# Kernel tuning notes

Measured on AMD Instinct MI355X. Metric: run time of the kernel, lower is better.

Reference implementation:

```python
import jax, jax.numpy as jnp
import numpy as np

B, T, H = 8, 512, 1024
DC = 8            # concept_dim_total = 6 + 2
DIN = H + DC      # 1032
V, L = 8, 4       # op_vocab_size, prog_len


def setup_inputs() -> dict:
    key = jax.random.key(0)
    ks = jax.random.split(key, 20)
    s = 0.02
    inp = {
        "x": jax.random.normal(ks[0], (B, T, H), dtype=jnp.float32),
        # concept classifier heads
        "W_tt": jax.random.normal(ks[1], (6, H), dtype=jnp.float32) * s,
        "b_tt": jnp.zeros((6,), jnp.float32),
        "W_pol": jax.random.normal(ks[2], (2, H), dtype=jnp.float32) * s,
        "b_pol": jnp.zeros((2,), jnp.float32),
        # program generator
        "W_c2h": jax.random.normal(ks[3], (H, DIN), dtype=jnp.float32) * s,
        "b_c2h": jnp.zeros((H,), jnp.float32),
        "W_ih": jax.random.normal(ks[4], (3 * H, DIN), dtype=jnp.float32) * s,
        "W_hh": jax.random.normal(ks[5], (3 * H, H), dtype=jnp.float32) * s,
        "b_ih": jnp.zeros((3 * H,), jnp.float32),
        "b_hh": jnp.zeros((3 * H,), jnp.float32),
        "W_proj": jax.random.normal(ks[6], (V, H), dtype=jnp.float32) * s,
        "b_proj": jnp.zeros((V,), jnp.float32),
        # op library: num_ops stacked Linear(DIN->H)-GELU-Linear(H->H)
        "W1": jax.random.normal(ks[7], (V, H, DIN), dtype=jnp.float32) * s,
        "b1": jnp.zeros((V, H), jnp.float32),
        "W2": jax.random.normal(ks[8], (V, H, H), dtype=jnp.float32) * s,
        "b2": jnp.zeros((V, H), jnp.float32),
    }
    return inp


def _forward(x, W_tt, b_tt, W_pol, b_pol, W_c2h, b_c2h, W_ih, W_hh, b_ih, b_hh,
             W_proj, b_proj, W1, b1, W2, b2):
    # concept classifier
    tt = x @ W_tt.T + b_tt              # (B,T,6)
    pol = x @ W_pol.T + b_pol           # (B,T,2)
    concept_feats = jnp.concatenate([tt, pol], axis=-1)  # (B,T,8)
    concept_summary = jnp.concatenate([tt.mean(axis=1), pol.mean(axis=1)], axis=-1)  # (B,8)
    pooled = x.mean(axis=1)             # (B,H)
    context = jnp.concatenate([pooled, concept_summary], axis=-1)  # (B,DIN)

    # program generator: GRU with zero inputs, h0 from context (PyTorch gate eqs)
    h0 = context @ W_c2h.T + b_c2h      # (B,H)
    zero_in = jnp.zeros((context.shape[0], DIN), x.dtype)
    gi = zero_in @ W_ih.T + b_ih        # (B,3H); zero-input contribution = bias
    gi_r, gi_z, gi_n = jnp.split(gi, 3, axis=-1)

    def gru_step(h, _):
        gh = h @ W_hh.T + b_hh
        gh_r, gh_z, gh_n = jnp.split(gh, 3, axis=-1)
        r = jax.nn.sigmoid(gi_r + gh_r)
        z = jax.nn.sigmoid(gi_z + gh_z)
        n = jnp.tanh(gi_n + r * gh_n)
        h_new = (1.0 - z) * n + z * h
        return h_new, h_new

    _, hs = jax.lax.scan(gru_step, h0, None, length=L)   # (L,B,H)
    rnn_out = jnp.transpose(hs, (1, 0, 2))               # (B,L,H)
    program_logits = rnn_out @ W_proj.T + b_proj         # (B,L,V)

    # op library: outputs are identical across L, so compute each op once and
    # average the softmax weights over L (exact same math as expand+mean).
    x_aug = jnp.concatenate([x, concept_feats], axis=-1)           # (B,T,DIN)
    hmid = jax.nn.gelu(jnp.einsum('btd,vhd->btvh', x_aug, W1) + b1, approximate=False)
    op_out = jnp.einsum('btvh,voh->btvo', hmid, W2) + b2           # (B,T,V,H)
    w = jax.nn.softmax(program_logits, axis=-1).mean(axis=1)       # (B,V)
    out = jnp.einsum('btvd,bv->btd', op_out, w)                    # (B,T,H)
    return out, program_logits, tt, pol, pooled


def reference(x, W_tt, b_tt, W_pol, b_pol, W_c2h, b_c2h, W_ih, W_hh, b_ih, b_hh,
              W_proj, b_proj, W1, b1, W2, b2):
    return _forward(x, W_tt, b_tt, W_pol, b_pol, W_c2h, b_c2h, W_ih, W_hh,
                    b_ih, b_hh, W_proj, b_proj, W1, b1, W2, b2)
```

## Files before the change

### kernel.cpp

```cpp
#include <hip/hip_runtime.h>
#include <hip/hip_bf16.h>
#include <math.h>

typedef __bf16 bf16;
typedef __bf16 bf16x8 __attribute__((ext_vector_type(8)));
typedef float f32x4 __attribute__((ext_vector_type(4)));


__device__ __forceinline__ float wsum(float v) {
#pragma unroll
  for (int off = 32; off; off >>= 1) v += __shfl_xor(v, off, 64);
  return v;
}

__device__ __forceinline__ void g2l16(const bf16* g, bf16* l) {
  __builtin_amdgcn_global_load_lds(
      (__attribute__((address_space(1))) void*)g,
      (__attribute__((address_space(3))) void*)l, 16, 0, 0);
}

__device__ __forceinline__ bf16x8 pack8(float4 a, float4 b) {
  bf16x8 r;
  r[0] = (bf16)a.x; r[1] = (bf16)a.y; r[2] = (bf16)a.z; r[3] = (bf16)a.w;
  r[4] = (bf16)b.x; r[5] = (bf16)b.y; r[6] = (bf16)b.z; r[7] = (bf16)b.w;
  return r;
}

__global__ void k_cvt(const float* __restrict__ s, bf16* __restrict__ d, long n) {
  long stride = (long)gridDim.x * blockDim.x;
  for (long i = (long)blockIdx.x * blockDim.x + threadIdx.x; i * 8 < n; i += stride) {
    long e = i * 8;
    if (e + 8 <= n) {
      float4 a = *(const float4*)(s + e);
      float4 b = *(const float4*)(s + e + 4);
      *(bf16x8*)(d + e) = pack8(a, b);
    } else {
      for (long j = e; j < n; j++) d[j] = (bf16)s[j];
    }
  }
}

__global__ void k_xext(const float* __restrict__ x, const float* __restrict__ feats,
                       bf16* __restrict__ xbE, int H, int KE, int DC, long BT) {
  int wave = threadIdx.x >> 6, lane = threadIdx.x & 63;
  long m = (long)blockIdx.x * 4 + wave;
  if (m >= BT) return;
  const float* xp = x + m * H;
  bf16* dp = xbE + m * KE;
  for (int e = lane * 8; e + 8 <= H; e += 512) {
    float4 a = *(const float4*)(xp + e);
    float4 b = *(const float4*)(xp + e + 4);
    *(bf16x8*)(dp + e) = pack8(a, b);
  }
  int pad = KE - H;
  if (lane < pad)
    dp[H + lane] = (lane < DC) ? (bf16)feats[m * DC + lane] : (bf16)0.f;
}

__global__ void k_w1ext(const float* __restrict__ W1, bf16* __restrict__ W1bE,
                        int H, int DIN, int KE, int DC, long N2) {
  int wave = threadIdx.x >> 6, lane = threadIdx.x & 63;
  long n = (long)blockIdx.x * 4 + wave;
  if (n >= N2) return;
  const float* sp = W1 + n * DIN;
  bf16* dp = W1bE + n * KE;
  for (int e = lane * 8; e + 8 <= H; e += 512) {
    float4 a = *(const float4*)(sp + e);
    float4 b = *(const float4*)(sp + e + 4);
    *(bf16x8*)(dp + e) = pack8(a, b);
  }
  int pad = KE - H;
  if (lane < pad)
    dp[H + lane] = (lane < DC) ? (bf16)sp[H + lane] : (bf16)0.f;
}

__global__ void k_init(float* __restrict__ outY, const float* __restrict__ wb2,
                       int H, int T, long BT) {
  int wave = threadIdx.x >> 6, lane = threadIdx.x & 63;
  long gm = (long)blockIdx.x * 4 + wave;
  if (gm >= BT) return;
  int b = (int)(gm / T);
  const float* s = wb2 + (size_t)b * H;
  float* d = outY + gm * H;
  for (int e = lane * 4; e + 4 <= H; e += 256)
    *(float4*)(d + e) = *(const float4*)(s + e);
}

template <int DCT>
__global__ void k_feats_t(const float* __restrict__ x,
                          const float* __restrict__ Wtt, const float* __restrict__ btt,
                          const float* __restrict__ Wpol, const float* __restrict__ bpol,
                          float* __restrict__ out_tt, float* __restrict__ out_pol,
                          float* __restrict__ feats,
                          int H, int T, int BT, int C1, int C2) {
  int wave = threadIdx.x >> 6, lane = threadIdx.x & 63;
  int site = blockIdx.x * 4 + wave;
  if (site >= BT) return;
  const float* xp = x + (size_t)site * H;
  const float* wp[DCT];
#pragma unroll
  for (int c = 0; c < DCT; c++)
    wp[c] = (c < C1) ? (Wtt + (size_t)c * H) : (Wpol + (size_t)(c - C1) * H);
  float acc[DCT];
#pragma unroll
  for (int c = 0; c < DCT; c++) acc[c] = 0.f;
  for (int k = lane * 4; k < H; k += 256) {
    float4 xv = *(const float4*)(xp + k);
#pragma unroll
    for (int c = 0; c < DCT; c++) {
      float4 wv4 = *(const float4*)(wp[c] + k);
      acc[c] += xv.x * wv4.x + xv.y * wv4.y + xv.z * wv4.z + xv.w * wv4.w;
    }
  }
#pragma unroll
  for (int c = 0; c < DCT; c++) acc[c] = wsum(acc[c]);
  if (lane == 0) {
#pragma unroll
    for (int c = 0; c < DCT; c++) {
      float val = acc[c] + (c < C1 ? btt[c] : bpol[c - C1]);
      if (c < C1) out_tt[(size_t)site * C1 + c] = val;
      else        out_pol[(size_t)site * C2 + (c - C1)] = val;
      feats[(size_t)site * DCT + c] = val;
    }
  }
}

__global__ void k_feats_g(const float* __restrict__ x,
                          const float* __restrict__ Wtt, const float* __restrict__ btt,
                          const float* __restrict__ Wpol, const float* __restrict__ bpol,
                          float* __restrict__ out_tt, float* __restrict__ out_pol,
                          float* __restrict__ feats,
                          int H, int T, int BT, int C1, int C2) {
  int wave = threadIdx.x >> 6, lane = threadIdx.x & 63;
  int site = blockIdx.x * 4 + wave;
  if (site >= BT) return;
  int DC = C1 + C2;
  const float* xp = x + (size_t)site * H;
  for (int c = 0; c < DC; c++) {
    const float* wr = (c < C1) ? (Wtt + (size_t)c * H) : (Wpol + (size_t)(c - C1) * H);
    float a = 0.f;
    for (int k = lane; k < H; k += 64) a += xp[k] * wr[k];
    a = wsum(a);
    if (lane == 0) {
      float val = a + (c < C1 ? btt[c] : bpol[c - C1]);
      if (c < C1) out_tt[(size_t)site * C1 + c] = val;
      else        out_pol[(size_t)site * C2 + (c - C1)] = val;
      feats[(size_t)site * DC + c] = val;
    }
  }
}

__global__ void k_fsum(const float* __restrict__ feats, float* __restrict__ fsum,
                       int T, int DC, int BDC) {
  int wave = threadIdx.x >> 6, lane = threadIdx.x & 63;
  int r = blockIdx.x * 4 + wave;
  if (r >= BDC) return;
  int b = r / DC, c = r % DC;
  const float* p = feats + ((size_t)b * T) * DC + c;
  float a = 0.f;
  for (int t = lane; t < T; t += 64) a += p[(size_t)t * DC];
  a = wsum(a);
  if (lane == 0) fsum[r] = a / (float)T;
}

__global__ void k_pool(const float* __restrict__ x, float* __restrict__ pooled,
                       int H, int T, int tsplit) {
  int hBlocks = (H + 255) / 256;
  int bs = blockIdx.x / tsplit, ts = blockIdx.x % tsplit;
  int b = bs / hBlocks;
  int h = (bs % hBlocks) * 256 + threadIdx.x;
  if (h >= H) return;
  int tlo = (int)(((long)T * ts) / tsplit), thi = (int)(((long)T * (ts + 1)) / tsplit);
  const float* p = x + (size_t)b * T * H + h;
  float s = 0.f;
  for (int t = tlo; t < thi; t++) s += p[(size_t)t * H];
  atomicAdd(&pooled[(size_t)b * H + h], s / (float)T);
}

__global__ void k_ctx_h0(const float* __restrict__ Wc2h, const float* __restrict__ bc2h,
                         const float* __restrict__ pooled, const float* __restrict__ fmean,
                         float* __restrict__ h0, float* __restrict__ out_pool,
                         int H, int DIN, int B, int DC) {
  int wave = threadIdx.x >> 6, lane = threadIdx.x & 63;
  int r = blockIdx.x * 4 + wave;
  if (r >= B * H) return;
  int b = r / H, j = r % H;
  const float* wrow = Wc2h + (size_t)j * DIN;
  float a = 0.f;
  for (int k = lane; k < DIN; k += 64) {
    float cv = (k < H) ? pooled[(size_t)b * H + k] : fmean[b * DC + (k - H)];
    a += cv * wrow[k];
  }
  a = wsum(a);
  if (lane == 0) {
    h0[r] = a + bc2h[j];
    out_pool[r] = pooled[r];
  }
}

__global__ void k_gru(const float* __restrict__ hin, const float* __restrict__ Whh,
                      const float* __restrict__ bih, const float* __restrict__ bhh,
                      float* __restrict__ hout, float* __restrict__ hsl,
                      int H, int B) {
  int wave = threadIdx.x >> 6, lane = threadIdx.x & 63;
  int r = blockIdx.x * 4 + wave;
  if (r >= B * H) return;
  int b = r / H, j = r % H;
  const float* h = hin + (size_t)b * H;
  const float* w0 = Whh + (size_t)j * H;
  const float* w1 = Whh + (size_t)(H + j) * H;
  const float* w2 = Whh + (size_t)(2 * H + j) * H;
  float ar = 0, az = 0, an = 0;
  for (int k = lane; k < H; k += 64) {
    float hv = h[k];
    ar += hv * w0[k];
    az += hv * w1[k];
    an += hv * w2[k];
  }
  ar = wsum(ar); az = wsum(az); an = wsum(an);
  if (lane == 0) {
    float ghr = ar + bhh[j];
    float ghz = az + bhh[H + j];
    float ghn = an + bhh[2 * H + j];
    float rg = 1.f / (1.f + expf(-(bih[j] + ghr)));
    float zg = 1.f / (1.f + expf(-(bih[H + j] + ghz)));
    float ng = tanhf(bih[2 * H + j] + rg * ghn);
    float hn = (1.f - zg) * ng + zg * h[j];
    hout[r] = hn;
    hsl[r] = hn;
  }
}

__global__ void k_logits(const float* __restrict__ hs, const float* __restrict__ Wproj,
                         const float* __restrict__ bproj, float* __restrict__ logits,
                         float* __restrict__ out_log, int H, int B, int L, int V) {
  int wave = threadIdx.x >> 6, lane = threadIdx.x & 63;
  int r = blockIdx.x * 4 + wave;
  if (r >= B * L * V) return;
  int b = r / (L * V), rem = r % (L * V), l = rem / V, u = rem % V;
  const float* h = hs + ((size_t)l * B + b) * H;
  const float* w = Wproj + (size_t)u * H;
  float a = 0.f;
  for (int k = lane; k < H; k += 64) a += h[k] * w[k];
  a = wsum(a);
  if (lane == 0) {
    a += bproj[u];
    int idx = (b * L + l) * V + u;
    logits[idx] = a;
    out_log[idx] = a;
  }
}

__global__ void k_wmix(const float* __restrict__ logits, const float* __restrict__ b2,
                       float* __restrict__ wv, float* __restrict__ wb2,
                       int B, int L, int V, int H) {
  __shared__ float sm[2048];
  __shared__ float wsh[512];
  int t = threadIdx.x;
  if (t < B * L) {
    const float* lg = logits + t * V;
    float mx = lg[0];
    for (int u = 1; u < V; u++) mx = fmaxf(mx, lg[u]);
    float s = 0.f;
    for (int u = 0; u < V; u++) s += expf(lg[u] - mx);
    for (int u = 0; u < V; u++) sm[t * V + u] = expf(lg[u] - mx) / s;
  }
  __syncthreads();
  if (t < B * V) {
    int b = t / V, u = t % V;
    float a = 0.f;
    for (int l = 0; l < L; l++) a += sm[(b * L + l) * V + u];
    a /= (float)L;
    wsh[t] = a;
    wv[t] = a;
  }
  __syncthreads();
  for (int idx = t; idx < B * H; idx += 256) {
    int b = idx / H, o = idx % H;
    float a = 0.f;
    for (int u = 0; u < V; u++) a += wsh[b * V + u] * b2[(size_t)u * H + o];
    wb2[idx] = a;
  }
}

__global__ __launch_bounds__(256, 2) void gemm1_mfma(
    const bf16* __restrict__ A, const bf16* __restrict__ Bb, bf16* __restrict__ hmid,
    const float* __restrict__ b1, const float* __restrict__ wv,
    int rows, long moff, int KE, int H, int N, int T, int V) {
  __shared__ __align__(16) bf16 As[128 * 32];
  __shared__ __align__(16) bf16 Bs[128 * 32];
  const int wave = threadIdx.x >> 6, lane = threadIdx.x & 63;
  const int m0 = blockIdx.y * 128, n0 = blockIdx.x * 128;
  const int mw = (wave >> 1) * 64, nw = (wave & 1) * 64;
  const int sRow = lane >> 2, sK = (lane & 3) * 8;
  const int rA = lane & 15, q8 = (lane >> 4) * 8;
  f32x4 acc[4][4];
#pragma unroll
  for (int i = 0; i < 4; i++)
#pragma unroll
    for (int j = 0; j < 4; j++) acc[i][j] = (f32x4){0.f, 0.f, 0.f, 0.f};

  int arow[2], brow[2];
#pragma unroll
  for (int t = 0; t < 2; ++t) {
    int s = wave * 2 + t;
    int r = s * 16 + sRow;
    arow[t] = (m0 + r < rows) ? (m0 + r) : (rows - 1);
    brow[t] = (n0 + r < N) ? (n0 + r) : (N - 1);
  }

  for (int k0 = 0; k0 < KE; k0 += 32) {
    __syncthreads();
#pragma unroll
    for (int t = 0; t < 2; ++t) {
      int s = wave * 2 + t;
      g2l16(A + (size_t)arow[t] * KE + k0 + sK, &As[s * 512]);
      g2l16(Bb + (size_t)brow[t] * KE + k0 + sK, &Bs[s * 512]);
    }
    __syncthreads();
    bf16x8 af[4], bf_[4];
#pragma unroll
    for (int i = 0; i < 4; i++) af[i] = *(const bf16x8*)&As[(mw + i * 16 + rA) * 32 + q8];
#pragma unroll
    for (int j = 0; j < 4; j++) bf_[j] = *(const bf16x8*)&Bs[(nw + j * 16 + rA) * 32 + q8];
#pragma unroll
    for (int i = 0; i < 4; i++)
#pragma unroll
      for (int j = 0; j < 4; j++)
        acc[i][j] = __builtin_amdgcn_mfma_f32_16x16x32_bf16(af[i], bf_[j], acc[i][j], 0, 0, 0);
  }

  int vj[4];
  float b1j[4];
#pragma unroll
  for (int j = 0; j < 4; j++) {
    int n = n0 + nw + j * 16 + rA;
    if (n >= N) n = N - 1;
    vj[j] = n / H;
    b1j[j] = b1[n];
  }
#pragma unroll
  for (int i = 0; i < 4; i++) {
#pragma unroll
    for (int r = 0; r < 4; r++) {
      int m = m0 + mw + i * 16 + (lane >> 4) * 4 + r;
      if (m >= rows) continue;
      long gm = moff + m;
      int b = (int)(gm / T);
#pragma unroll
      for (int j = 0; j < 4; j++) {
        int n = n0 + nw + j * 16 + rA;
        if (n >= N) continue;
        float val = acc[i][j][r] + b1j[j];
        val = 0.5f * val * (1.0f + erff(val * 0.70710678118654752f));
        val *= wv[b * V + vj[j]];
        hmid[(size_t)m * N + n] = (bf16)val;
      }
    }
  }
}

__global__ __launch_bounds__(256, 2) void gemm2_mfma(
    const bf16* __restrict__ A, const bf16* __restrict__ W2b, float* __restrict__ outY,
    int rows, long moff, int H, int K, int T, int kchunk) {
  __shared__ __align__(16) bf16 As[128 * 32];
  __shared__ __align__(16) bf16 Bs[128 * 32];
  const int wave = threadIdx.x >> 6, lane = threadIdx.x & 63;
  const int m0 = blockIdx.y * 128, n0 = blockIdx.x * 128;
  const int mw = (wave >> 1) * 64, nw = (wave & 1) * 64;
  const int sRow = lane >> 2, sK = (lane & 3) * 8;
  const int rA = lane & 15, q8 = (lane >> 4) * 8;
  int kz0 = blockIdx.z * kchunk;
  int kz1 = kz0 + kchunk; if (kz1 > K) kz1 = K;
  if (kz0 >= K) return;
  f32x4 acc[4][4];
#pragma unroll
  for (int i = 0; i < 4; i++)
#pragma unroll
    for (int j = 0; j < 4; j++) acc[i][j] = (f32x4){0.f, 0.f, 0.f, 0.f};

  int arow[2], brow[2];
#pragma unroll
  for (int t = 0; t < 2; ++t) {
    int s = wave * 2 + t;
    int r = s * 16 + sRow;
    arow[t] = (m0 + r < rows) ? (m0 + r) : (rows - 1);
    brow[t] = (n0 + r < H) ? (n0 + r) : (H - 1);
  }

  int kv = kz0 / H, kh = kz0 % H;
  for (int k0 = kz0; k0 < kz1; k0 += 32) {
    const bf16* Bk = W2b + (size_t)kv * H * H + kh;
    __syncthreads();
#pragma unroll
    for (int t = 0; t < 2; ++t) {
      int s = wave * 2 + t;
      g2l16(A + (size_t)arow[t] * K + k0 + sK, &As[s * 512]);
      g2l16(Bk + (size_t)brow[t] * H + sK, &Bs[s * 512]);
    }
    __syncthreads();
    bf16x8 af[4], bf_[4];
#pragma unroll
    for (int i = 0; i < 4; i++) af[i] = *(const bf16x8*)&As[(mw + i * 16 + rA) * 32 + q8];
#pragma unroll
    for (int j = 0; j < 4; j++) bf_[j] = *(const bf16x8*)&Bs[(nw + j * 16 + rA) * 32 + q8];
#pragma unroll
    for (int i = 0; i < 4; i++)
#pragma unroll
      for (int j = 0; j < 4; j++)
        acc[i][j] = __builtin_amdgcn_mfma_f32_16x16x32_bf16(af[i], bf_[j], acc[i][j], 0, 0, 0);
    kh += 32;
    if (kh >= H) { kh = 0; kv++; }
  }

#pragma unroll
  for (int i = 0; i < 4; i++) {
#pragma unroll
    for (int r = 0; r < 4; r++) {
      int m = m0 + mw + i * 16 + (lane >> 4) * 4 + r;
      if (m >= rows) continue;
      long gm = moff + m;
#pragma unroll
      for (int j = 0; j < 4; j++) {
        int n = n0 + nw + j * 16 + rA;
        if (n >= H) continue;
        atomicAdd(&outY[(size_t)gm * H + n], acc[i][j][r]);
      }
    }
  }
}

extern "C" void kernel_launch(void* const* d_in, const int* in_sizes, int n_in,
                              void* d_out, int out_size, void* d_ws, size_t ws_size,
                              hipStream_t stream) {
  const float* x      = (const float*)d_in[0];
  const float* W_tt   = (const float*)d_in[1];
  const float* b_tt   = (const float*)d_in[2];
  const float* W_pol  = (const float*)d_in[3];
  const float* b_pol  = (const float*)d_in[4];
  const float* W_c2h  = (const float*)d_in[5];
  const float* b_c2h  = (const float*)d_in[6];
  const float* W_hh   = (const float*)d_in[8];
  const float* b_ih   = (const float*)d_in[9];
  const float* b_hh   = (const float*)d_in[10];
  const float* W_proj = (const float*)d_in[11];
  const float* b_proj = (const float*)d_in[12];
  const float* W1     = (const float*)d_in[13];
  const float* b1     = (const float*)d_in[14];
  const float* W2     = (const float*)d_in[15];
  const float* b2     = (const float*)d_in[16];
  float* out = (float*)d_out;
  char* ws = (char*)d_ws;

  const int C1 = in_sizes[2];
  const int C2 = in_sizes[4];
  const int H  = in_sizes[1] / C1;
  const int DC = C1 + C2;
  const int DIN = H + DC;
  const int V  = in_sizes[12];
  const long BT = (long)in_sizes[0] / H;
  long R = (long)out_size - BT * (long)(H + DC);
  int B = 0, L = 0;
  for (int Lc = 1; Lc <= 32; ++Lc) {
    long den = (long)Lc * V + H;
    if (R % den == 0) {
      long Bc = R / den;
      if (Bc >= 1 && BT % Bc == 0) {
        if (B == 0 || Lc == 4) { B = (int)Bc; L = Lc; }
        if (Lc == 4) break;
      }
    }
  }
  if (B == 0) { B = 8; L = 4; }
  const int T = (int)(BT / B);
  const long N2 = (long)V * H;
  const int KE = H + 32;

  size_t o = 0;
  auto alloc = [&](size_t bytes) { size_t r = o; o = (o + bytes + 255) & ~(size_t)255; return r; };
  float* feats  = (float*)(ws + alloc((size_t)BT * DC * 4));
  size_t off_pooled = alloc((size_t)B * H * 4);
  float* pooled = (float*)(ws + off_pooled);
  size_t off_fsum = alloc((size_t)B * DC * 4);
  float* fsum   = (float*)(ws + off_fsum);
  float* hbuf   = (float*)(ws + alloc((size_t)2 * B * H * 4));
  float* hs     = (float*)(ws + alloc((size_t)L * B * H * 4));
  float* logits = (float*)(ws + alloc((size_t)B * L * V * 4));
  float* wv     = (float*)(ws + alloc((size_t)B * V * 4));
  float* wb2    = (float*)(ws + alloc((size_t)B * H * 4));
  bf16* xbE  = (bf16*)(ws + alloc((size_t)BT * KE * 2));
  bf16* W1bE = (bf16*)(ws + alloc((size_t)N2 * KE * 2));
  bf16* W2b  = (bf16*)(ws + alloc((size_t)N2 * H * 2));
  size_t off_hmid = alloc(0);
  long avail = (long)ws_size - (long)off_hmid;
  long mcMax = avail / (N2 * 2);
  long Mc = (mcMax / 128) * 128;
  long bt128 = ((BT + 127) / 128) * 128;
  if (Mc > bt128) Mc = bt128;
  if (Mc < 128) Mc = 128;
  bf16* hmid = (bf16*)(ws + off_hmid);

  float* out_y    = out;
  float* out_log  = out_y + (size_t)BT * H;
  float* out_tt   = out_log + (size_t)B * L * V;
  float* out_pol  = out_tt + (size_t)BT * C1;
  float* out_pool = out_pol + (size_t)BT * C2;

  hipMemsetAsync(ws + off_pooled, 0, (size_t)B * H * 4, stream);

  k_cvt<<<4096, 256, 0, stream>>>(W2, W2b, N2 * (long)H);
  if (DC == 8 && (H & 1023) == 0)
    k_feats_t<8><<<(int)((BT + 3) / 4), 256, 0, stream>>>(x, W_tt, b_tt, W_pol, b_pol,
                                                          out_tt, out_pol, feats,
                                                          H, T, (int)BT, C1, C2);
  else
    k_feats_g<<<(int)((BT + 3) / 4), 256, 0, stream>>>(x, W_tt, b_tt, W_pol, b_pol,
                                                       out_tt, out_pol, feats,
                                                       H, T, (int)BT, C1, C2);
  k_fsum<<<(B * DC + 3) / 4, 256, 0, stream>>>(feats, fsum, T, DC, B * DC);
  k_xext<<<(int)((BT + 3) / 4), 256, 0, stream>>>(x, feats, xbE, H, KE, DC, BT);
  k_w1ext<<<(int)((N2 + 3) / 4), 256, 0, stream>>>(W1, W1bE, H, DIN, KE, DC, N2);
  int hBlocks = (H + 255) / 256;
  k_pool<<<B * hBlocks * 8, 256, 0, stream>>>(x, pooled, H, T, 8);
  k_ctx_h0<<<(B * H + 3) / 4, 256, 0, stream>>>(W_c2h, b_c2h, pooled, fsum,
                                                hbuf, out_pool, H, DIN, B, DC);
  float* hA = hbuf;
  float* hB = hbuf + (size_t)B * H;
  for (int l = 0; l < L; ++l) {
    k_gru<<<(B * H + 3) / 4, 256, 0, stream>>>((l & 1) ? hB : hA, W_hh, b_ih, b_hh,
                                               (l & 1) ? hA : hB, hs + (size_t)l * B * H,
                                               H, B);
  }
  k_logits<<<(B * L * V + 3) / 4, 256, 0, stream>>>(hs, W_proj, b_proj, logits,
                                                    out_log, H, B, L, V);
  k_wmix<<<1, 256, 0, stream>>>(logits, b2, wv, wb2, B, L, V, H);
  k_init<<<(int)((BT + 3) / 4), 256, 0, stream>>>(out_y, wb2, H, T, BT);

  const int ZS = 4;
  int kchunk = (int)((((N2 / ZS) + 31) / 32) * 32);
  for (long moff = 0; moff < BT; moff += Mc) {
    int rows = (int)(((BT - moff) < Mc) ? (BT - moff) : Mc);
    dim3 g1((unsigned)((N2 + 127) / 128), (unsigned)((rows + 127) / 128));
    dim3 g2((unsigned)((H + 127) / 128), (unsigned)((rows + 127) / 128), ZS);
    gemm1_mfma<<<g1, 256, 0, stream>>>(xbE + (size_t)moff * KE, W1bE, hmid, b1, wv,
                                       rows, moff, KE, H, (int)N2, T, V);
    gemm2_mfma<<<g2, 256, 0, stream>>>(hmid, W2b, out_y,
                                       rows, moff, H, (int)N2, T, kchunk);
  }
}
```

Before: 535.0 us.

## Double GEMM K-tile to 64 with XOR-swizzled LDS, XCD remap, split-K partial buffers

Both MFMA GEMMs now stage 64-wide K tiles into LDS with an XOR swizzle, which halves the number of barrier pairs per K and aims to cut LDS bank conflicts. Block indices are remapped so that tiles sharing operands land on the same XCD, for better L2 reuse. The split-K GEMM2 no longer uses fp32 atomicAdd into the output. It writes per-split partials that a new reduction kernel sums together with the bias term, which replaces the old init kernel. In exchange there is extra workspace and memory traffic for the partials, plus one more launch per chunk. KE padding grows to H+64.

Measured after the change: 459.0 us. -14.2%, faster.

```diff
diff --git a/kernel.cpp b/kernel.cpp
--- a/kernel.cpp
+++ b/kernel.cpp
@@ -72,18 +72,6 @@
   int pad = KE - H;
   if (lane < pad)
     dp[H + lane] = (lane < DC) ? (bf16)sp[H + lane] : (bf16)0.f;
-}
-
-__global__ void k_init(float* __restrict__ outY, const float* __restrict__ wb2,
-                       int H, int T, long BT) {
-  int wave = threadIdx.x >> 6, lane = threadIdx.x & 63;
-  long gm = (long)blockIdx.x * 4 + wave;
-  if (gm >= BT) return;
-  int b = (int)(gm / T);
-  const float* s = wb2 + (size_t)b * H;
-  float* d = outY + gm * H;
-  for (int e = lane * 4; e + 4 <= H; e += 256)
-    *(float4*)(d + e) = *(const float4*)(s + e);
 }
 
 template <int DCT>
@@ -287,47 +275,64 @@
     const bf16* __restrict__ A, const bf16* __restrict__ Bb, bf16* __restrict__ hmid,
     const float* __restrict__ b1, const float* __restrict__ wv,
     int rows, long moff, int KE, int H, int N, int T, int V) {
-  __shared__ __align__(16) bf16 As[128 * 32];
-  __shared__ __align__(16) bf16 Bs[128 * 32];
+  __shared__ __align__(16) bf16 As[128 * 64];
+  __shared__ __align__(16) bf16 Bs[128 * 64];
   const int wave = threadIdx.x >> 6, lane = threadIdx.x & 63;
-  const int m0 = blockIdx.y * 128, n0 = blockIdx.x * 128;
+  int bx = blockIdx.x, by = blockIdx.y;
+  if (gridDim.x == 64 && (gridDim.y & 3) == 0) {
+    int f = by * 64 + bx;
+    int xcd = f & 7, q = f >> 3;
+    int cs = q >> 5, t = q & 31;
+    bx = xcd * 8 + (t & 7);
+    by = cs * 4 + (t >> 3);
+  }
+  const int m0 = by * 128, n0 = bx * 128;
   const int mw = (wave >> 1) * 64, nw = (wave & 1) * 64;
-  const int sRow = lane >> 2, sK = (lane & 3) * 8;
-  const int rA = lane & 15, q8 = (lane >> 4) * 8;
+  const int rr = lane >> 3;
+  const int srcOff = ((lane & 7) ^ rr) << 3;
+  const int rA = lane & 15, q4 = lane >> 4;
   f32x4 acc[4][4];
 #pragma unroll
   for (int i = 0; i < 4; i++)
 #pragma unroll
     for (int j = 0; j < 4; j++) acc[i][j] = (f32x4){0.f, 0.f, 0.f, 0.f};
 
-  int arow[2], brow[2];
-#pragma unroll
-  for (int t = 0; t < 2; ++t) {
-    int s = wave * 2 + t;
-    int r = s * 16 + sRow;
+  int arow[4], brow[4];
+#pragma unroll
+  for (int t = 0; t < 4; ++t) {
+    int r = wave * 32 + t * 8 + rr;
     arow[t] = (m0 + r < rows) ? (m0 + r) : (rows - 1);
     brow[t] = (n0 + r < N) ? (n0 + r) : (N - 1);
   }
 
-  for (int k0 = 0; k0 < KE; k0 += 32) {
+  for (int k0 = 0; k0 < KE; k0 += 64) {
     __syncthreads();
 #pragma unroll
-    for (int t = 0; t < 2; ++t) {
-      int s = wave * 2 + t;
-      g2l16(A + (size_t)arow[t] * KE + k0 + sK, &As[s * 512]);
-      g2l16(Bb + (size_t)brow[t] * KE + k0 + sK, &Bs[s * 512]);
+    for (int t = 0; t < 4; ++t) {
+      int c = wave * 4 + t;
+      g2l16(A + (size_t)arow[t] * KE + k0 + srcOff, &As[c * 512]);
+      g2l16(Bb + (size_t)brow[t] * KE + k0 + srcOff, &Bs[c * 512]);
     }
     __syncthreads();
-    bf16x8 af[4], bf_[4];
-#pragma unroll
-    for (int i = 0; i < 4; i++) af[i] = *(const bf16x8*)&As[(mw + i * 16 + rA) * 32 + q8];
-#pragma unroll
-    for (int j = 0; j < 4; j++) bf_[j] = *(const bf16x8*)&Bs[(nw + j * 16 + rA) * 32 + q8];
-#pragma unroll
-    for (int i = 0; i < 4; i++)
-#pragma unroll
-      for (int j = 0; j < 4; j++)
-        acc[i][j] = __builtin_amdgcn_mfma_f32_16x16x32_bf16(af[i], bf_[j], acc[i][j], 0, 0, 0);
+#pragma unroll
+    for (int kk = 0; kk < 2; ++kk) {
+      bf16x8 af[4], bfr[4];
+#pragma unroll
+      for (int i = 0; i < 4; i++) {
+        int row = mw + i * 16 + rA;
+        af[i] = *(const bf16x8*)&As[row * 64 + ((((kk << 2) + q4) ^ (row & 7)) << 3)];
+      }
+#pragma unroll
+      for (int j = 0; j < 4; j++) {
+        int row = nw + j * 16 + rA;
+        bfr[j] = *(const bf16x8*)&Bs[row * 64 + ((((kk << 2) + q4) ^ (row & 7)) << 3)];
+      }
+#pragma unroll
+      for (int i = 0; i < 4; i++)
+#pragma unroll
+        for (int j = 0; j < 4; j++)
+          acc[i][j] = __builtin_amdgcn_mfma_f32_16x16x32_bf16(af[i], bfr[j], acc[i][j], 0, 0, 0);
+    }
   }
 
   int vj[4];
@@ -343,7 +348,7 @@
   for (int i = 0; i < 4; i++) {
 #pragma unroll
     for (int r = 0; r < 4; r++) {
-      int m = m0 + mw + i * 16 + (lane >> 4) * 4 + r;
+      int m = m0 + mw + i * 16 + q4 * 4 + r;
       if (m >= rows) continue;
       long gm = moff + m;
       int b = (int)(gm / T);
@@ -361,15 +366,24 @@
 }
 
 __global__ __launch_bounds__(256, 2) void gemm2_mfma(
-    const bf16* __restrict__ A, const bf16* __restrict__ W2b, float* __restrict__ outY,
-    int rows, long moff, int H, int K, int T, int kchunk) {
-  __shared__ __align__(16) bf16 As[128 * 32];
-  __shared__ __align__(16) bf16 Bs[128 * 32];
+    const bf16* __restrict__ A, const bf16* __restrict__ W2b, float* __restrict__ part,
+    long partStride, int rows, int H, int K, int kchunk) {
+  __shared__ __align__(16) bf16 As[128 * 64];
+  __shared__ __align__(16) bf16 Bs[128 * 64];
   const int wave = threadIdx.x >> 6, lane = threadIdx.x & 63;
-  const int m0 = blockIdx.y * 128, n0 = blockIdx.x * 128;
+  int bx = blockIdx.x, by = blockIdx.y;
+  if (gridDim.x == 8 && (gridDim.y & 31) == 0) {
+    int f = by * 8 + bx;
+    int xcd = f & 7, q = f >> 3;
+    int cs = q >> 5, t = q & 31;
+    bx = t & 7;
+    by = (xcd + (cs << 3)) * 4 + (t >> 3);
+  }
+  const int m0 = by * 128, n0 = bx * 128;
   const int mw = (wave >> 1) * 64, nw = (wave & 1) * 64;
-  const int sRow = lane >> 2, sK = (lane & 3) * 8;
-  const int rA = lane & 15, q8 = (lane >> 4) * 8;
+  const int rr = lane >> 3;
+  const int srcOff = ((lane & 7) ^ rr) << 3;
+  const int rA = lane & 15, q4 = lane >> 4;
   int kz0 = blockIdx.z * kchunk;
   int kz1 = kz0 + kchunk; if (kz1 > K) kz1 = K;
   if (kz0 >= K) return;
@@ -379,54 +393,82 @@
 #pragma unroll
     for (int j = 0; j < 4; j++) acc[i][j] = (f32x4){0.f, 0.f, 0.f, 0.f};
 
-  int arow[2], brow[2];
-#pragma unroll
-  for (int t = 0; t < 2; ++t) {
-    int s = wave * 2 + t;
-    int r = s * 16 + sRow;
+  int arow[4], brow[4];
+#pragma unroll
+  for (int t = 0; t < 4; ++t) {
+    int r = wave * 32 + t * 8 + rr;
     arow[t] = (m0 + r < rows) ? (m0 + r) : (rows - 1);
     brow[t] = (n0 + r < H) ? (n0 + r) : (H - 1);
   }
 
   int kv = kz0 / H, kh = kz0 % H;
-  for (int k0 = kz0; k0 < kz1; k0 += 32) {
+  for (int k0 = kz0; k0 < kz1; k0 += 64) {
     const bf16* Bk = W2b + (size_t)kv * H * H + kh;
     __syncthreads();
 #pragma unroll
-    for (int t = 0; t < 2; ++t) {
-      int s = wave * 2 + t;
-      g2l16(A + (size_t)arow[t] * K + k0 + sK, &As[s * 512]);
-      g2l16(Bk + (size_t)brow[t] * H + sK, &Bs[s * 512]);
+    for (int t = 0; t < 4; ++t) {
+      int c = wave * 4 + t;
+      g2l16(A + (size_t)arow[t] * K + k0 + srcOff, &As[c * 512]);
+      g2l16(Bk + (size_t)brow[t] * H + srcOff, &Bs[c * 512]);
     }
     __syncthreads();
-    bf16x8 af[4], bf_[4];
-#pragma unroll
-    for (int i = 0; i < 4; i++) af[i] = *(const bf16x8*)&As[(mw + i * 16 + rA) * 32 + q8];
-#pragma unroll
-    for (int j = 0; j < 4; j++) bf_[j] = *(const bf16x8*)&Bs[(nw + j * 16 + rA) * 32 + q8];
-#pragma unroll
-    for (int i = 0; i < 4; i++)
-#pragma unroll
-      for (int j = 0; j < 4; j++)
-        acc[i][j] = __builtin_amdgcn_mfma_f32_16x16x32_bf16(af[i], bf_[j], acc[i][j], 0, 0, 0);
-    kh += 32;
+#pragma unroll
+    for (int kk = 0; kk < 2; ++kk) {
+      bf16x8 af[4], bfr[4];
+#pragma unroll
+      for (int i = 0; i < 4; i++) {
+        int row = mw + i * 16 + rA;
+        af[i] = *(const bf16x8*)&As[row * 64 + ((((kk << 2) + q4) ^ (row & 7)) << 3)];
+      }
+#pragma unroll
+      for (int j = 0; j < 4; j++) {
+        int row = nw + j * 16 + rA;
+        bfr[j] = *(const bf16x8*)&Bs[row * 64 + ((((kk << 2) + q4) ^ (row & 7)) << 3)];
+      }
+#pragma unroll
+      for (int i = 0; i < 4; i++)
+#pragma unroll
+        for (int j = 0; j < 4; j++)
+          acc[i][j] = __builtin_amdgcn_mfma_f32_16x16x32_bf16(af[i], bfr[j], acc[i][j], 0, 0, 0);
+    }
+    kh += 64;
     if (kh >= H) { kh = 0; kv++; }
   }
 
+  float* pz = part + (size_t)blockIdx.z * partStride;
 #pragma unroll
   for (int i = 0; i < 4; i++) {
 #pragma unroll
     for (int r = 0; r < 4; r++) {
-      int m = m0 + mw + i * 16 + (lane >> 4) * 4 + r;
+      int m = m0 + mw + i * 16 + q4 * 4 + r;
       if (m >= rows) continue;
-      long gm = moff + m;
 #pragma unroll
       for (int j = 0; j < 4; j++) {
         int n = n0 + nw + j * 16 + rA;
         if (n >= H) continue;
-        atomicAdd(&outY[(size_t)gm * H + n], acc[i][j][r]);
-      }
-    }
+        pz[(size_t)m * H + n] = acc[i][j][r];
+      }
+    }
+  }
+}
+
+__global__ void k_red(const float* __restrict__ part, const float* __restrict__ wb2,
+                      float* __restrict__ outY, long moff, int rows, long partStride,
+                      int H, int T, int ZS) {
+  int wave = threadIdx.x >> 6, lane = threadIdx.x & 63;
+  long m = (long)blockIdx.x * 4 + wave;
+  if (m >= rows) return;
+  long gm = moff + m;
+  int b = (int)(gm / T);
+  const float* w = wb2 + (size_t)b * H;
+  float* d = outY + (size_t)gm * H;
+  for (int e = lane * 4; e + 4 <= H; e += 256) {
+    float4 s = *(const float4*)(w + e);
+    for (int z = 0; z < ZS; z++) {
+      float4 p = *(const float4*)(part + (size_t)z * partStride + (size_t)m * H + e);
+      s.x += p.x; s.y += p.y; s.z += p.z; s.w += p.w;
+    }
+    *(float4*)(d + e) = s;
   }
 }
 
@@ -474,15 +516,15 @@
   if (B == 0) { B = 8; L = 4; }
   const int T = (int)(BT / B);
   const long N2 = (long)V * H;
-  const int KE = H + 32;
+  const int KE = H + 64;
+  const int ZS = 4;
 
   size_t o = 0;
   auto alloc = [&](size_t bytes) { size_t r = o; o = (o + bytes + 255) & ~(size_t)255; return r; };
   float* feats  = (float*)(ws + alloc((size_t)BT * DC * 4));
   size_t off_pooled = alloc((size_t)B * H * 4);
   float* pooled = (float*)(ws + off_pooled);
-  size_t off_fsum = alloc((size_t)B * DC * 4);
-  float* fsum   = (float*)(ws + off_fsum);
+  float* fsum   = (float*)(ws + alloc((size_t)B * DC * 4));
   float* hbuf   = (float*)(ws + alloc((size_t)2 * B * H * 4));
   float* hs     = (float*)(ws + alloc((size_t)L * B * H * 4));
   float* logits = (float*)(ws + alloc((size_t)B * L * V * 4));
@@ -492,13 +534,15 @@
   bf16* W1bE = (bf16*)(ws + alloc((size_t)N2 * KE * 2));
   bf16* W2b  = (bf16*)(ws + alloc((size_t)N2 * H * 2));
   size_t off_hmid = alloc(0);
+  long rowBytes = N2 * 2 + (long)ZS * H * 4;
   long avail = (long)ws_size - (long)off_hmid;
-  long mcMax = avail / (N2 * 2);
-  long Mc = (mcMax / 128) * 128;
+  long Mc = ((avail / rowBytes) / 128) * 128;
   long bt128 = ((BT + 127) / 128) * 128;
   if (Mc > bt128) Mc = bt128;
   if (Mc < 128) Mc = 128;
   bf16* hmid = (bf16*)(ws + off_hmid);
+  float* part = (float*)(ws + off_hmid + (size_t)Mc * N2 * 2);
+  long partStride = Mc * (long)H;
 
   float* out_y    = out;
   float* out_log  = out_y + (size_t)BT * H;
@@ -534,17 +578,17 @@
   k_logits<<<(B * L * V + 3) / 4, 256, 0, stream>>>(hs, W_proj, b_proj, logits,
                                                     out_log, H, B, L, V);
   k_wmix<<<1, 256, 0, stream>>>(logits, b2, wv, wb2, B, L, V, H);
-  k_init<<<(int)((BT + 3) / 4), 256, 0, stream>>>(out_y, wb2, H, T, BT);
-
-  const int ZS = 4;
-  int kchunk = (int)((((N2 / ZS) + 31) / 32) * 32);
+
+  int kchunk = (int)((((N2 / ZS) + 63) / 64) * 64);
   for (long moff = 0; moff < BT; moff += Mc) {
     int rows = (int)(((BT - moff) < Mc) ? (BT - moff) : Mc);
     dim3 g1((unsigned)((N2 + 127) / 128), (unsigned)((rows + 127) / 128));
     dim3 g2((unsigned)((H + 127) / 128), (unsigned)((rows + 127) / 128), ZS);
     gemm1_mfma<<<g1, 256, 0, stream>>>(xbE + (size_t)moff * KE, W1bE, hmid, b1, wv,
                                        rows, moff, KE, H, (int)N2, T, V);
-    gemm2_mfma<<<g2, 256, 0, stream>>>(hmid, W2b, out_y,
-                                       rows, moff, H, (int)N2, T, kchunk);
-  }
-}
+    gemm2_mfma<<<g2, 256, 0, stream>>>(hmid, W2b, part, partStride,
+                                       rows, H, (int)N2, kchunk);
+    k_red<<<(int)((rows + 3) / 4), 256, 0, stream>>>(part, wb2, out_y, moff, rows,
+                                                     partStride, H, T, ZS);
+  }
+}
```
